# Optimization experiments

Hardware: AMD Instinct MI355X
Metric: run time of the kernel (lower is better)

Reference implementation:

```python
import jax, jax.numpy as jnp
import numpy as np

L = 5           # num_layer
D = 128         # emb_dim
N = 100_000     # num nodes
E = 1_600_000   # num edges
EDGE_F = 7      # raw edge feature dim
BN_EPS = 1e-5


def batchnorm(z, gamma, beta):
    # BatchNorm1d in training-style normalization: biased batch mean/var over axis 0
    mu = z.mean(axis=0)
    var = z.var(axis=0)
    return gamma * (z - mu) * jax.lax.rsqrt(var + BN_EPS) + beta


def setup_inputs() -> dict:
    key = jax.random.key(0)
    ks = jax.random.split(key, 16)
    s = 0.05
    return {
        "x": jnp.zeros((N,), jnp.int32),                               # Embedding(1, D) indices
        "edge_index": jax.random.randint(ks[0], (2, E), 0, N, jnp.int32),
        "edge_attr": jax.random.normal(ks[1], (E, EDGE_F), jnp.float32),
        "node_emb": jax.random.normal(ks[2], (1, D), jnp.float32) * s,
        "We": jax.random.normal(ks[3], (L, EDGE_F, D), jnp.float32) * s,   # edge_encoder weight
        "be": jax.random.normal(ks[4], (L, D), jnp.float32) * s,
        "eps": jnp.zeros((L,), jnp.float32),                               # GIN eps, init 0
        "W1": jax.random.normal(ks[5], (L, D, 2 * D), jnp.float32) * s,
        "b1": jax.random.normal(ks[6], (L, 2 * D), jnp.float32) * s,
        "g1": jnp.ones((L, 2 * D), jnp.float32),                           # mlp inner BN gamma
        "bt1": jnp.zeros((L, 2 * D), jnp.float32),                         # mlp inner BN beta
        "W2": jax.random.normal(ks[7], (L, 2 * D, D), jnp.float32) * s,
        "b2": jax.random.normal(ks[8], (L, D), jnp.float32) * s,
        "gbn": jnp.ones((L, D), jnp.float32),                              # outer BN gamma
        "bbn": jnp.zeros((L, D), jnp.float32),                             # outer BN beta
    }


def reference(x, edge_index, edge_attr, node_emb, We, be, eps, W1, b1, g1, bt1, W2, b2, gbn, bbn):
    # node encoder (Embedding with vocab=1)
    h = node_emb[x]                       # [N, D]
    src, dst = edge_index[0], edge_index[1]
    for l in range(L):
        # edge embedding + GIN message: relu(x_j + edge_emb), scatter-add at dst
        ee = edge_attr @ We[l] + be[l]                       # [E, D]
        msg = jax.nn.relu(h[src] + ee)                       # gather + add + relu
        agg = jax.ops.segment_sum(msg, dst, num_segments=N)  # scatter-add
        out = (1.0 + eps[l]) * h + agg                       # [N, D]
        # mlp: Linear(D,2D) -> BN -> ReLU -> Linear(2D,D)
        z = batchnorm(out @ W1[l] + b1[l], g1[l], bt1[l])
        z = jax.nn.relu(z) @ W2[l] + b2[l]
        # outer BatchNorm; dropout is identity in eval mode
        h = batchnorm(z, gbn[l], bbn[l])
        if l < L - 1:
            h = jax.nn.relu(h)
    return h
```

## Files before the change

kernel.cpp:

```cpp
#include <hip/hip_runtime.h>
#include <cstddef>

#define NN 100000
#define NE 1600000
#define D 128
#define D2 256
#define EF 7
#define NL 5
#define BN_EPS 1e-5f
#define GW 12500
#define SCAN_NB ((NN + 1023) / 1024)

typedef unsigned short ushort_t;
typedef __attribute__((ext_vector_type(8))) _Float16 f16x8;
typedef __attribute__((ext_vector_type(2))) _Float16 h2v;
typedef __attribute__((ext_vector_type(4))) float f32x4;

__device__ __forceinline__ void atomAddF(float* p, float v) { unsafeAtomicAdd(p, v); }

__device__ __forceinline__ ushort_t f2h(float f) {
    return __builtin_bit_cast(ushort_t, (_Float16)f);
}
__device__ __forceinline__ unsigned pk2h(float lo, float hi) {
    return (unsigned)f2h(lo) | ((unsigned)f2h(hi) << 16);
}
__device__ __forceinline__ float h2f(unsigned u16) {
    return (float)__builtin_bit_cast(_Float16, (ushort_t)(u16 & 0xFFFFu));
}
__device__ __forceinline__ h2v u2h2(unsigned u) { return __builtin_bit_cast(h2v, u); }

__global__ __launch_bounds__(256)
void hist_kernel(const int* __restrict__ ei, int* __restrict__ counts)
{
    const int e = blockIdx.x * 256 + threadIdx.x;
    if (e < NE) atomicAdd(&counts[ei[NE + e]], 1);
}

__global__ __launch_bounds__(256)
void scanA_kernel(const int* __restrict__ counts, int* __restrict__ bsum)
{
    __shared__ int sred[256];
    const int t = threadIdx.x;
    const int base = blockIdx.x * 1024 + t * 4;
    int s = 0;
    #pragma unroll
    for (int j = 0; j < 4; ++j) { const int i = base + j; if (i < NN) s += counts[i]; }
    sred[t] = s;
    __syncthreads();
    for (int off = 128; off > 0; off >>= 1) {
        if (t < off) sred[t] += sred[t + off];
        __syncthreads();
    }
    if (t == 0) bsum[blockIdx.x] = sred[0];
}

__global__ __launch_bounds__(128)
void scanB_kernel(const int* __restrict__ bsum, int* __restrict__ bbase,
                  int* __restrict__ offs)
{
    __shared__ int ss[128];
    const int t = threadIdx.x;
    const int v = (t < SCAN_NB) ? bsum[t] : 0;
    ss[t] = v;
    __syncthreads();
    for (int off = 1; off < 128; off <<= 1) {
        int u = 0;
        if (t >= off) u = ss[t - off];
        __syncthreads();
        ss[t] += u;
        __syncthreads();
    }
    if (t < SCAN_NB) bbase[t] = ss[t] - v;
    if (t == 0) offs[NN] = NE;
}

__global__ __launch_bounds__(256)
void scanC_kernel(const int* __restrict__ counts, const int* __restrict__ bbase,
                  int* __restrict__ offs, int* __restrict__ offmut)
{
    __shared__ int sts[256];
    const int t = threadIdx.x;
    const int base = blockIdx.x * 1024 + t * 4;
    int c[4];
    int s = 0;
    #pragma unroll
    for (int j = 0; j < 4; ++j) {
        const int i = base + j;
        c[j] = (i < NN) ? counts[i] : 0;
        s += c[j];
    }
    sts[t] = s;
    __syncthreads();
    for (int off = 1; off < 256; off <<= 1) {
        int u = 0;
        if (t >= off) u = sts[t - off];
        __syncthreads();
        sts[t] += u;
        __syncthreads();
    }
    int run = bbase[blockIdx.x] + sts[t] - s;
    #pragma unroll
    for (int j = 0; j < 4; ++j) {
        const int i = base + j;
        if (i < NN) { offs[i] = run; offmut[i] = run; run += c[j]; }
    }
}

__global__ __launch_bounds__(256)
void scatter_kernel(const int* __restrict__ ei, const float* __restrict__ ea,
                    int* __restrict__ offmut, int* __restrict__ sSrc,
                    ushort_t* __restrict__ eaH)
{
    const int e = blockIdx.x * 256 + threadIdx.x;
    if (e < NE) {
        const int dst = ei[NE + e];
        const int pos = atomicAdd(&offmut[dst], 1);
        sSrc[pos] = ei[e];
        const float* eap = &ea[(size_t)e * EF];
        const unsigned o0 = pk2h(eap[0], eap[1]);
        const unsigned o1 = pk2h(eap[2], eap[3]);
        const unsigned o2 = pk2h(eap[4], eap[5]);
        const unsigned o3 = pk2h(eap[6], 0.f);
        *(uint4*)&eaH[(size_t)pos * 8] = make_uint4(o0, o1, o2, o3);
    }
}

__global__ __launch_bounds__(256)
void wconv_kernel(const float* __restrict__ W1, const float* __restrict__ W2,
                  ushort_t* __restrict__ W1t, ushort_t* __restrict__ W2t)
{
    const int idx = blockIdx.x * 256 + threadIdx.x;
    const int per = D * D2;
    if (idx < NL * per) {
        const int l = idx / per, r = idx % per;
        const int k1 = r / D2, n1 = r % D2;
        W1t[(size_t)l * per + n1 * D + k1] = f2h(W1[idx]);
        const int k2 = r / D, n2 = r % D;
        W2t[(size_t)l * per + n2 * D2 + k2] = f2h(W2[idx]);
    }
}

template<int L0>
__global__ __launch_bounds__(256)
void gather_kernel(const int* __restrict__ offs, const int* __restrict__ sSrc,
                   const ushort_t* __restrict__ eaH,
                   const float* __restrict__ We, const float* __restrict__ be,
                   const ushort_t* __restrict__ z2H, const float* __restrict__ stats2p,
                   const float* __restrict__ gbn, const float* __restrict__ bbn,
                   const float* __restrict__ h0, const float* __restrict__ epsp,
                   ushort_t* __restrict__ xinH, float* __restrict__ xsum)
{
    __shared__ __align__(16) float sCS[4][D];
    const int lane = threadIdx.x & 63;
    const int w = threadIdx.x >> 6;
    const int wid = blockIdx.x * 4 + w;

    const float2* We2 = (const float2*)We;
    const unsigned* hU = (const unsigned*)z2H;
    unsigned* xU = (unsigned*)xinH;
    h2v wP[EF];
    #pragma unroll
    for (int k = 0; k < EF; ++k) {
        const float2 wf = We2[k * 64 + lane];
        wP[k] = (h2v){(_Float16)wf.x, (_Float16)wf.y};
    }
    h2v beP;
    {
        const float2 bf = ((const float2*)be)[lane];
        beP = (h2v){(_Float16)bf.x, (_Float16)bf.y};
    }
    float2 h0v = {0.f, 0.f};
    h2v h0P = (h2v){(_Float16)0.f, (_Float16)0.f};
    h2v aP = (h2v){(_Float16)0.f, (_Float16)0.f};
    h2v cP = (h2v){(_Float16)0.f, (_Float16)0.f};
    if (L0) {
        h0v = ((const float2*)h0)[lane];
        h0P = (h2v){(_Float16)h0v.x, (_Float16)h0v.y};
    } else {
        const float inv = 1.0f / (float)NN;
        const int c0i = 2 * lane, c1i = 2 * lane + 1;
        const float mu0 = stats2p[c0i] * inv;
        const float mu1 = stats2p[c1i] * inv;
        const float v0 = fmaf(-mu0, mu0, stats2p[D + c0i] * inv);
        const float v1 = fmaf(-mu1, mu1, stats2p[D + c1i] * inv);
        const float a0 = gbn[c0i] * rsqrtf(v0 + BN_EPS);
        const float a1 = gbn[c1i] * rsqrtf(v1 + BN_EPS);
        const float c0 = fmaf(-a0, mu0, bbn[c0i]);
        const float c1 = fmaf(-a1, mu1, bbn[c1i]);
        aP = (h2v){(_Float16)a0, (_Float16)a1};
        cP = (h2v){(_Float16)c0, (_Float16)c1};
    }
    const float epsv = 1.0f + *epsp;
    const h2v zz = (h2v){(_Float16)0.f, (_Float16)0.f};

    int p4[8], e4[8];
    #pragma unroll
    for (int i = 0; i < 8; ++i) {
        const int n = wid + i * GW;
        p4[i] = __builtin_amdgcn_readfirstlane(offs[n]);
        e4[i] = __builtin_amdgcn_readfirstlane(offs[n + 1]);
    }
    int mx = 0;
    #pragma unroll
    for (int i = 0; i < 8; ++i) mx = max(mx, e4[i] - p4[i]);

    float2 acc[8];
    #pragma unroll
    for (int i = 0; i < 8; ++i) acc[i] = (float2){0.f, 0.f};

    for (int j = 0; j < mx; ++j) {
        unsigned hwd[8];
        uint4 ev4[8];
        bool on[8];
        #pragma unroll
        for (int i = 0; i < 8; ++i) {
            on[i] = p4[i] < e4[i];
            if (on[i]) {
                ev4[i] = *(const uint4*)&eaH[(size_t)p4[i] * 8];
                if (!L0) {
                    const int src = sSrc[p4[i]];
                    hwd[i] = hU[(src << 6) + lane];
                }
            }
        }
        #pragma unroll
        for (int i = 0; i < 8; ++i) {
            if (on[i]) {
                const h2v e01 = u2h2(ev4[i].x);
                const h2v e23 = u2h2(ev4[i].y);
                const h2v e45 = u2h2(ev4[i].z);
                const h2v e6x = u2h2(ev4[i].w);
                h2v m = beP;
                m = __builtin_elementwise_fma(__builtin_shufflevector(e01, e01, 0, 0), wP[0], m);
                m = __builtin_elementwise_fma(__builtin_shufflevector(e01, e01, 1, 1), wP[1], m);
                m = __builtin_elementwise_fma(__builtin_shufflevector(e23, e23, 0, 0), wP[2], m);
                m = __builtin_elementwise_fma(__builtin_shufflevector(e23, e23, 1, 1), wP[3], m);
                m = __builtin_elementwise_fma(__builtin_shufflevector(e45, e45, 0, 0), wP[4], m);
                m = __builtin_elementwise_fma(__builtin_shufflevector(e45, e45, 1, 1), wP[5], m);
                m = __builtin_elementwise_fma(__builtin_shufflevector(e6x, e6x, 0, 0), wP[6], m);
                h2v hh;
                if (L0) hh = h0P;
                else hh = __builtin_elementwise_max(
                         __builtin_elementwise_fma(aP, u2h2(hwd[i]), cP), zz);
                const h2v r = __builtin_elementwise_max(m + hh, zz);
                acc[i].x += (float)r.x;
                acc[i].y += (float)r.y;
                ++p4[i];
            }
        }
    }

    float2 cs = {0.f, 0.f};
    #pragma unroll
    for (int i = 0; i < 8; ++i) {
        const int n = wid + i * GW;
        float2 hs;
        if (L0) hs = h0v;
        else {
            const h2v hz = __builtin_elementwise_max(
                __builtin_elementwise_fma(aP, u2h2(hU[(n << 6) + lane]), cP), zz);
            hs.x = (float)hz.x; hs.y = (float)hz.y;
        }
        float2 a = acc[i];
        a.x = fmaf(epsv, hs.x, a.x);
        a.y = fmaf(epsv, hs.y, a.y);
        cs.x += a.x; cs.y += a.y;
        xU[(n << 6) + lane] = pk2h(a.x, a.y);
    }
    sCS[w][2 * lane] = cs.x;
    sCS[w][2 * lane + 1] = cs.y;
    __syncthreads();
    if (threadIdx.x < D) {
        atomAddF(&xsum[threadIdx.x],
                 sCS[0][threadIdx.x] + sCS[1][threadIdx.x] +
                 sCS[2][threadIdx.x] + sCS[3][threadIdx.x]);
    }
}

__global__ __launch_bounds__(256, 2)
void mm1_kernel(const ushort_t* __restrict__ xinH, const float* __restrict__ xsum,
                const ushort_t* __restrict__ W1t,
                ushort_t* __restrict__ z1H, float* __restrict__ stats)
{
    __shared__ __align__(16) ushort_t sA[64 * 256];
    __shared__ __align__(16) float sM[D];
    const int t = threadIdx.x;
    if (t < D) sM[t] = xsum[t] * (1.0f / (float)NN);
    const int i0 = blockIdx.x * 64;
    const int lane = t & 63, w = t >> 6;
    const int nb = w * 64;

    f16x8 bfr[4][4];
    #pragma unroll
    for (int nt = 0; nt < 4; ++nt)
        #pragma unroll
        for (int ks = 0; ks < 4; ++ks) {
            const int n = nb + nt * 16 + (lane & 15);
            const int k = ks * 32 + (lane >> 4) * 8;
            bfr[nt][ks] = *(const f16x8*)&W1t[n * D + k];
        }
    __syncthreads();

    #pragma unroll
    for (int p = 0; p < 4; ++p) {
        const int linear = p * 256 + t;
        const int row = linear >> 4, ch = linear & 15;
        const int gi = i0 + row;
        unsigned oo[4] = {0, 0, 0, 0};
        if (gi < NN) {
            const uint4 v = *(const uint4*)&xinH[(size_t)gi * D + ch * 8];
            const unsigned uu[4] = {v.x, v.y, v.z, v.w};
            #pragma unroll
            for (int j2 = 0; j2 < 4; ++j2) {
                const int c0 = ch * 8 + j2 * 2;
                oo[j2] = pk2h(h2f(uu[j2]) - sM[c0], h2f(uu[j2] >> 16) - sM[c0 + 1]);
            }
        }
        unsigned boff = (unsigned)(row * 256 + ch * 16);
        boff ^= (unsigned)((row & 7) << 4);
        *(uint4*)((char*)sA + boff) = make_uint4(oo[0], oo[1], oo[2], oo[3]);
    }
    __syncthreads();

    f32x4 acc[4][4];
    #pragma unroll
    for (int a = 0; a < 4; ++a)
        #pragma unroll
        for (int b = 0; b < 4; ++b) acc[a][b] = (f32x4){0.f, 0.f, 0.f, 0.f};

    #pragma unroll
    for (int mt = 0; mt < 4; ++mt) {
        f16x8 af[4];
        #pragma unroll
        for (int ks = 0; ks < 4; ++ks) {
            const int row = mt * 16 + (lane & 15);
            unsigned boff = (unsigned)(row * 256 + ks * 64 + (lane >> 4) * 16);
            boff ^= (unsigned)((row & 7) << 4);
            af[ks] = *(const f16x8*)((const char*)sA + boff);
        }
        #pragma unroll
        for (int nt = 0; nt < 4; ++nt)
            #pragma unroll
            for (int ks = 0; ks < 4; ++ks)
                acc[mt][nt] = __builtin_amdgcn_mfma_f32_16x16x32_f16(af[ks], bfr[nt][ks], acc[mt][nt], 0, 0, 0);
    }

    float s[4], q[4];
    #pragma unroll
    for (int nt = 0; nt < 4; ++nt) { s[nt] = 0.f; q[nt] = 0.f; }
    #pragma unroll
    for (int nt = 0; nt < 4; ++nt)
        #pragma unroll
        for (int mt = 0; mt < 4; ++mt)
            #pragma unroll
            for (int r = 0; r < 4; ++r) {
                const int i = i0 + mt * 16 + (lane >> 4) * 4 + r;
                if (i < NN) {
                    const float v = acc[mt][nt][r];
                    s[nt] += v; q[nt] = fmaf(v, v, q[nt]);
                }
            }
    #pragma unroll
    for (int nt = 0; nt < 4; ++nt) {
        s[nt] += __shfl_xor(s[nt], 16, 64); s[nt] += __shfl_xor(s[nt], 32, 64);
        q[nt] += __shfl_xor(q[nt], 16, 64); q[nt] += __shfl_xor(q[nt], 32, 64);
    }
    if (lane < 16) {
        #pragma unroll
        for (int nt = 0; nt < 4; ++nt) {
            const int n = nb + nt * 16 + lane;
            atomAddF(&stats[n], s[nt]);
            atomAddF(&stats[D2 + n], q[nt]);
        }
    }

    __syncthreads();
    #pragma unroll
    for (int nt = 0; nt < 4; ++nt)
        #pragma unroll
        for (int mt = 0; mt < 4; ++mt)
            #pragma unroll
            for (int r = 0; r < 4; ++r) {
                const int row = mt * 16 + (lane >> 4) * 4 + r;
                const int col = nb + nt * 16 + (lane & 15);
                const unsigned byte = (unsigned)(row * 512 + col * 2) ^ ((unsigned)(row & 7) << 4);
                *(ushort_t*)((char*)sA + byte) = f2h(acc[mt][nt][r]);
            }
    __syncthreads();
    {
        const int row = t >> 2;
        const int gi = i0 + row;
        const int cb = (t & 3) * 64;
        if (gi < NN) {
            #pragma unroll
            for (int c = 0; c < 8; ++c) {
                const unsigned byte = (unsigned)(row * 512 + (cb + c * 8) * 2) ^ ((unsigned)(row & 7) << 4);
                const uint4 v = *(const uint4*)((const char*)sA + byte);
                *(uint4*)&z1H[(size_t)gi * D2 + cb + c * 8] = v;
            }
        }
    }
}

__global__ __launch_bounds__(256, 2)
void mm2_kernel(const ushort_t* __restrict__ z1H, const float* __restrict__ stats1,
                const float* __restrict__ g1, const float* __restrict__ bt1,
                const ushort_t* __restrict__ W2t,
                ushort_t* __restrict__ z2H, float* __restrict__ stats2)
{
    __shared__ __align__(16) ushort_t sA[64 * 256];
    __shared__ __align__(16) float sAff[2 * D2];
    __shared__ __align__(16) float sYm[D2];
    const int t = threadIdx.x;
    {
        const float inv = 1.0f / (float)NN;
        const float mu = stats1[t] * inv;
        const float var = fmaf(-mu, mu, stats1[D2 + t] * inv);
        const float a = g1[t] * rsqrtf(var + BN_EPS);
        sAff[t] = a;
        sAff[D2 + t] = fmaf(-a, mu, bt1[t]);
        const float m0 = bt1[t];
        const float sg = fabsf(g1[t]);
        float ym;
        if (sg > 1e-20f) {
            const float r = m0 / sg;
            const float Ph = 0.5f * (1.0f + erff(r * 0.70710678f));
            const float ph = 0.39894228f * expf(-0.5f * r * r);
            ym = m0 * Ph + sg * ph;
        } else {
            ym = fmaxf(m0, 0.f);
        }
        sYm[t] = ym;
    }
    const int i0 = blockIdx.x * 64;
    const int lane = t & 63, w = t >> 6;
    const int nb = w * 32;

    f16x8 bfr[2][8];
    #pragma unroll
    for (int nt = 0; nt < 2; ++nt)
        #pragma unroll
        for (int ks = 0; ks < 8; ++ks) {
            const int n = nb + nt * 16 + (lane & 15);
            const int k = ks * 32 + (lane >> 4) * 8;
            bfr[nt][ks] = *(const f16x8*)&W2t[n * D2 + k];
        }
    __syncthreads();

    #pragma unroll
    for (int p = 0; p < 8; ++p) {
        const int linear = p * 256 + t;
        const int row = linear >> 5, ch = linear & 31;
        const int gi = i0 + row;
        unsigned oo[4] = {0, 0, 0, 0};
        if (gi < NN) {
            const uint4 v = *(const uint4*)&z1H[(size_t)gi * D2 + ch * 8];
            const unsigned uu[4] = {v.x, v.y, v.z, v.w};
            #pragma unroll
            for (int j2 = 0; j2 < 4; ++j2) {
                const int c0 = ch * 8 + j2 * 2;
                float lo = h2f(uu[j2]);
                float hi = h2f(uu[j2] >> 16);
                lo = fmaxf(fmaf(sAff[c0], lo, sAff[D2 + c0]), 0.f) - sYm[c0];
                hi = fmaxf(fmaf(sAff[c0 + 1], hi, sAff[D2 + c0 + 1]), 0.f) - sYm[c0 + 1];
                oo[j2] = pk2h(lo, hi);
            }
        }
        unsigned boff = (unsigned)(row * 512 + ch * 16);
        boff ^= (unsigned)((row & 7) << 4);
        *(uint4*)((char*)sA + boff) = make_uint4(oo[0], oo[1], oo[2], oo[3]);
    }
    __syncthreads();

    f32x4 acc[4][2];
    #pragma unroll
    for (int a = 0; a < 4; ++a)
        #pragma unroll
        for (int b = 0; b < 2; ++b) acc[a][b] = (f32x4){0.f, 0.f, 0.f, 0.f};

    #pragma unroll
    for (int mt = 0; mt < 4; ++mt) {
        f16x8 af[8];
        #pragma unroll
        for (int ks = 0; ks < 8; ++ks) {
            const int row = mt * 16 + (lane & 15);
            unsigned boff = (unsigned)(row * 512 + ks * 64 + (lane >> 4) * 16);
            boff ^= (unsigned)((row & 7) << 4);
            af[ks] = *(const f16x8*)((const char*)sA + boff);
        }
        #pragma unroll
        for (int nt = 0; nt < 2; ++nt)
            #pragma unroll
            for (int ks = 0; ks < 8; ++ks)
                acc[mt][nt] = __builtin_amdgcn_mfma_f32_16x16x32_f16(af[ks], bfr[nt][ks], acc[mt][nt], 0, 0, 0);
    }

    float s[2], q[2];
    #pragma unroll
    for (int nt = 0; nt < 2; ++nt) { s[nt] = 0.f; q[nt] = 0.f; }
    #pragma unroll
    for (int nt = 0; nt < 2; ++nt)
        #pragma unroll
        for (int mt = 0; mt < 4; ++mt)
            #pragma unroll
            for (int r = 0; r < 4; ++r) {
                const int i = i0 + mt * 16 + (lane >> 4) * 4 + r;
                if (i < NN) {
                    const float v = acc[mt][nt][r];
                    s[nt] += v; q[nt] = fmaf(v, v, q[nt]);
                }
            }
    #pragma unroll
    for (int nt = 0; nt < 2; ++nt) {
        s[nt] += __shfl_xor(s[nt], 16, 64); s[nt] += __shfl_xor(s[nt], 32, 64);
        q[nt] += __shfl_xor(q[nt], 16, 64); q[nt] += __shfl_xor(q[nt], 32, 64);
    }
    if (lane < 16) {
        #pragma unroll
        for (int nt = 0; nt < 2; ++nt) {
            const int n = nb + nt * 16 + lane;
            atomAddF(&stats2[n], s[nt]);
            atomAddF(&stats2[D + n], q[nt]);
        }
    }

    __syncthreads();
    #pragma unroll
    for (int nt = 0; nt < 2; ++nt)
        #pragma unroll
        for (int mt = 0; mt < 4; ++mt)
            #pragma unroll
            for (int r = 0; r < 4; ++r) {
                const int row = mt * 16 + (lane >> 4) * 4 + r;
                const int col = nb + nt * 16 + (lane & 15);
                const unsigned byte = (unsigned)(row * 256 + col * 2) ^ ((unsigned)(row & 7) << 4);
                *(ushort_t*)((char*)sA + byte) = f2h(acc[mt][nt][r]);
            }
    __syncthreads();
    {
        const int row = t >> 2;
        const int gi = i0 + row;
        const int cb = (t & 3) * 32;
        if (gi < NN) {
            #pragma unroll
            for (int c = 0; c < 4; ++c) {
                const unsigned byte = (unsigned)(row * 256 + (cb + c * 8) * 2) ^ ((unsigned)(row & 7) << 4);
                const uint4 v = *(const uint4*)((const char*)sA + byte);
                *(uint4*)&z2H[(size_t)gi * D + cb + c * 8] = v;
            }
        }
    }
}

__global__ __launch_bounds__(256)
void act_kernel(const ushort_t* __restrict__ z2H, const float* __restrict__ stats2,
                const float* __restrict__ g, const float* __restrict__ bt,
                float* __restrict__ out)
{
    __shared__ float sA[D], sC[D];
    const int t = threadIdx.x;
    if (t < D) {
        const float inv = 1.0f / (float)NN;
        const float mu = stats2[t] * inv;
        const float var = fmaf(-mu, mu, stats2[D + t] * inv);
        const float a = g[t] * rsqrtf(var + BN_EPS);
        sA[t] = a;
        sC[t] = fmaf(-a, mu, bt[t]);
    }
    __syncthreads();
    const int idx = blockIdx.x * 256 + t;
    if (idx < NN * D / 4) {
        const int d0 = (idx * 4) & (D - 1);
        const uint2 v = *(const uint2*)&z2H[(size_t)idx * 4];
        float4 o;
        o.x = fmaf(sA[d0 + 0], h2f(v.x),       sC[d0 + 0]);
        o.y = fmaf(sA[d0 + 1], h2f(v.x >> 16), sC[d0 + 1]);
        o.z = fmaf(sA[d0 + 2], h2f(v.y),       sC[d0 + 2]);
        o.w = fmaf(sA[d0 + 3], h2f(v.y >> 16), sC[d0 + 3]);
        *(float4*)&out[(size_t)idx * 4] = o;
    }
}

extern "C" void kernel_launch(void* const* d_in, const int* in_sizes, int n_in,
                              void* d_out, int out_size, void* d_ws, size_t ws_size,
                              hipStream_t stream)
{
    (void)in_sizes; (void)n_in; (void)out_size; (void)ws_size;
    const int*   ei       = (const int*)d_in[1];
    const float* ea       = (const float*)d_in[2];
    const float* node_emb = (const float*)d_in[3];
    const float* We       = (const float*)d_in[4];
    const float* be       = (const float*)d_in[5];
    const float* eps      = (const float*)d_in[6];
    const float* W1       = (const float*)d_in[7];
    const float* g1       = (const float*)d_in[9];
    const float* bt1      = (const float*)d_in[10];
    const float* W2       = (const float*)d_in[11];
    const float* gbn      = (const float*)d_in[13];
    const float* bbn      = (const float*)d_in[14];
    float* out = (float*)d_out;

    char* base = (char*)d_ws;
    size_t off = 0;
    auto alloc = [&](size_t bytes) -> void* {
        void* p = base + off;
        off = (off + bytes + 255) & ~(size_t)255;
        return p;
    };
    ushort_t* xinH   = (ushort_t*)alloc((size_t)NN * D * 2);
    ushort_t* z1H    = (ushort_t*)alloc((size_t)NN * D2 * 2);
    ushort_t* z2H    = (ushort_t*)alloc((size_t)NN * D * 2);
    ushort_t* W1t    = (ushort_t*)alloc((size_t)NL * D * D2 * 2);
    ushort_t* W2t    = (ushort_t*)alloc((size_t)NL * D * D2 * 2);
    float*    red    = (float*)alloc((size_t)NL * 896 * sizeof(float));
    int*      counts = (int*)alloc((NN + 1) * sizeof(int));
    int*      offs   = (int*)alloc((NN + 1) * sizeof(int));
    int*      offmut = (int*)alloc(NN * sizeof(int));
    int*      bsum   = (int*)alloc(SCAN_NB * sizeof(int));
    int*      bbase  = (int*)alloc(SCAN_NB * sizeof(int));
    int*      sSrc   = (int*)alloc((size_t)NE * sizeof(int));
    ushort_t* eaH    = (ushort_t*)alloc((size_t)NE * 8 * 2);

    hipMemsetAsync(counts, 0, (NN + 1) * sizeof(int), stream);
    hipMemsetAsync(red, 0, (size_t)NL * 896 * sizeof(float), stream);
    hist_kernel<<<(NE + 255) / 256, 256, 0, stream>>>(ei, counts);
    scanA_kernel<<<SCAN_NB, 256, 0, stream>>>(counts, bsum);
    scanB_kernel<<<1, 128, 0, stream>>>(bsum, bbase, offs);
    scanC_kernel<<<SCAN_NB, 256, 0, stream>>>(counts, bbase, offs, offmut);
    scatter_kernel<<<(NE + 255) / 256, 256, 0, stream>>>(ei, ea, offmut, sSrc, eaH);
    wconv_kernel<<<(NL * D * D2 + 255) / 256, 256, 0, stream>>>(W1, W2, W1t, W2t);

    for (int l = 0; l < NL; ++l) {
        float* redl   = red + (size_t)l * 896;
        float* stats1 = redl;
        float* stats2 = redl + 512;
        float* xsum   = redl + 768;
        if (l == 0) {
            gather_kernel<1><<<GW / 4, 256, 0, stream>>>(offs, sSrc, eaH,
                We + l * EF * D, be + l * D,
                z2H, nullptr, nullptr, nullptr,
                node_emb, eps + l, xinH, xsum);
        } else {
            const float* stats2p = red + (size_t)(l - 1) * 896 + 512;
            gather_kernel<0><<<GW / 4, 256, 0, stream>>>(offs, sSrc, eaH,
                We + l * EF * D, be + l * D,
                z2H, stats2p, gbn + (l - 1) * D, bbn + (l - 1) * D,
                node_emb, eps + l, xinH, xsum);
        }
        mm1_kernel<<<(NN + 63) / 64, 256, 0, stream>>>(xinH, xsum, W1t + (size_t)l * D * D2,
                                                       z1H, stats1);
        mm2_kernel<<<(NN + 63) / 64, 256, 0, stream>>>(z1H, stats1, g1 + l * D2, bt1 + l * D2,
                                                       W2t + (size_t)l * D * D2,
                                                       z2H, stats2);
    }
    act_kernel<<<(NN * D / 4 + 255) / 256, 256, 0, stream>>>(
        z2H, red + (size_t)(NL - 1) * 896 + 512, gbn + (NL - 1) * D, bbn + (NL - 1) * D, out);
}
```

Baseline: 1.560 ms.

## Sort nodes by in-degree so each gather wave handles similar-degree nodes

Adds a counting sort of nodes by in-degree (capped at 64 buckets) that builds a permutation. Each gather wave now takes 8 consecutive nodes from the sorted order, so the per-wave loop bound set by the largest degree wastes fewer idle iterations. Wave indices are scrambled with a multiplicative hash so heavy and light groups spread across blocks. The cost is three small preprocessing kernels plus one more indirection, and node reads and writes become scattered instead of strided.

Result: slower. 1.716 ms (+10.0%).

```diff
diff --git a/kernel.cpp b/kernel.cpp
--- a/kernel.cpp
+++ b/kernel.cpp
@@ -10,6 +10,7 @@
 #define BN_EPS 1e-5f
 #define GW 12500
 #define SCAN_NB ((NN + 1023) / 1024)
+#define DB 64
 
 typedef unsigned short ushort_t;
 typedef __attribute__((ext_vector_type(8))) _Float16 f16x8;
@@ -103,6 +104,65 @@
     for (int j = 0; j < 4; ++j) {
         const int i = base + j;
         if (i < NN) { offs[i] = run; offmut[i] = run; run += c[j]; }
+    }
+}
+
+__global__ __launch_bounds__(256)
+void dhistL_kernel(const int* __restrict__ counts, int* __restrict__ bh)
+{
+    __shared__ int lh[DB];
+    const int t = threadIdx.x;
+    if (t < DB) lh[t] = 0;
+    __syncthreads();
+    const int base = blockIdx.x * 1024 + t * 4;
+    #pragma unroll
+    for (int j = 0; j < 4; ++j) {
+        const int i = base + j;
+        if (i < NN) atomicAdd(&lh[min(counts[i], DB - 1)], 1);
+    }
+    __syncthreads();
+    if (t < DB) bh[t * SCAN_NB + blockIdx.x] = lh[t];
+}
+
+__global__ __launch_bounds__(DB)
+void dscan2_kernel(const int* __restrict__ bh, int* __restrict__ gb)
+{
+    __shared__ int tot[DB];
+    __shared__ int gdb[DB];
+    const int d = threadIdx.x;
+    int run = 0;
+    for (int b = 0; b < SCAN_NB; ++b) run += bh[d * SCAN_NB + b];
+    tot[d] = run;
+    __syncthreads();
+    if (d == 0) {
+        int r = 0;
+        for (int k = 0; k < DB; ++k) { gdb[k] = r; r += tot[k]; }
+    }
+    __syncthreads();
+    run = gdb[d];
+    for (int b = 0; b < SCAN_NB; ++b) {
+        const int v = bh[d * SCAN_NB + b];
+        gb[d * SCAN_NB + b] = run;
+        run += v;
+    }
+}
+
+__global__ __launch_bounds__(256)
+void dpermL_kernel(const int* __restrict__ counts, const int* __restrict__ gb,
+                   int* __restrict__ perm)
+{
+    __shared__ int cur[DB];
+    const int t = threadIdx.x;
+    if (t < DB) cur[t] = gb[t * SCAN_NB + blockIdx.x];
+    __syncthreads();
+    const int base = blockIdx.x * 1024 + t * 4;
+    #pragma unroll
+    for (int j = 0; j < 4; ++j) {
+        const int i = base + j;
+        if (i < NN) {
+            const int r = atomicAdd(&cur[min(counts[i], DB - 1)], 1);
+            perm[r] = i;
+        }
     }
 }
 
@@ -143,7 +203,7 @@
 template<int L0>
 __global__ __launch_bounds__(256)
 void gather_kernel(const int* __restrict__ offs, const int* __restrict__ sSrc,
-                   const ushort_t* __restrict__ eaH,
+                   const ushort_t* __restrict__ eaH, const int* __restrict__ perm,
                    const float* __restrict__ We, const float* __restrict__ be,
                    const ushort_t* __restrict__ z2H, const float* __restrict__ stats2p,
                    const float* __restrict__ gbn, const float* __restrict__ bbn,
@@ -154,6 +214,7 @@
     const int lane = threadIdx.x & 63;
     const int w = threadIdx.x >> 6;
     const int wid = blockIdx.x * 4 + w;
+    const int wids = (int)(((long long)wid * 9973) % GW);
 
     const float2* We2 = (const float2*)We;
     const unsigned* hU = (const unsigned*)z2H;
@@ -193,12 +254,12 @@
     const float epsv = 1.0f + *epsp;
     const h2v zz = (h2v){(_Float16)0.f, (_Float16)0.f};
 
-    int p4[8], e4[8];
+    int nd[8], p4[8], e4[8];
     #pragma unroll
     for (int i = 0; i < 8; ++i) {
-        const int n = wid + i * GW;
-        p4[i] = __builtin_amdgcn_readfirstlane(offs[n]);
-        e4[i] = __builtin_amdgcn_readfirstlane(offs[n + 1]);
+        nd[i] = __builtin_amdgcn_readfirstlane(perm[wids * 8 + i]);
+        p4[i] = __builtin_amdgcn_readfirstlane(offs[nd[i]]);
+        e4[i] = __builtin_amdgcn_readfirstlane(offs[nd[i] + 1]);
     }
     int mx = 0;
     #pragma unroll
@@ -253,7 +314,7 @@
     float2 cs = {0.f, 0.f};
     #pragma unroll
     for (int i = 0; i < 8; ++i) {
-        const int n = wid + i * GW;
+        const int n = nd[i];
         float2 hs;
         if (L0) hs = h0v;
         else {
@@ -618,6 +679,9 @@
     int*      offmut = (int*)alloc(NN * sizeof(int));
     int*      bsum   = (int*)alloc(SCAN_NB * sizeof(int));
     int*      bbase  = (int*)alloc(SCAN_NB * sizeof(int));
+    int*      bh     = (int*)alloc((size_t)DB * SCAN_NB * sizeof(int));
+    int*      gb     = (int*)alloc((size_t)DB * SCAN_NB * sizeof(int));
+    int*      perm   = (int*)alloc(NN * sizeof(int));
     int*      sSrc   = (int*)alloc((size_t)NE * sizeof(int));
     ushort_t* eaH    = (ushort_t*)alloc((size_t)NE * 8 * 2);
 
@@ -627,6 +691,9 @@
     scanA_kernel<<<SCAN_NB, 256, 0, stream>>>(counts, bsum);
     scanB_kernel<<<1, 128, 0, stream>>>(bsum, bbase, offs);
     scanC_kernel<<<SCAN_NB, 256, 0, stream>>>(counts, bbase, offs, offmut);
+    dhistL_kernel<<<SCAN_NB, 256, 0, stream>>>(counts, bh);
+    dscan2_kernel<<<1, DB, 0, stream>>>(bh, gb);
+    dpermL_kernel<<<SCAN_NB, 256, 0, stream>>>(counts, gb, perm);
     scatter_kernel<<<(NE + 255) / 256, 256, 0, stream>>>(ei, ea, offmut, sSrc, eaH);
     wconv_kernel<<<(NL * D * D2 + 255) / 256, 256, 0, stream>>>(W1, W2, W1t, W2t);
 
@@ -636,13 +703,13 @@
         float* stats2 = redl + 512;
         float* xsum   = redl + 768;
         if (l == 0) {
-            gather_kernel<1><<<GW / 4, 256, 0, stream>>>(offs, sSrc, eaH,
+            gather_kernel<1><<<GW / 4, 256, 0, stream>>>(offs, sSrc, eaH, perm,
                 We + l * EF * D, be + l * D,
                 z2H, nullptr, nullptr, nullptr,
                 node_emb, eps + l, xinH, xsum);
         } else {
             const float* stats2p = red + (size_t)(l - 1) * 896 + 512;
-            gather_kernel<0><<<GW / 4, 256, 0, stream>>>(offs, sSrc, eaH,
+            gather_kernel<0><<<GW / 4, 256, 0, stream>>>(offs, sSrc, eaH, perm,
                 We + l * EF * D, be + l * D,
                 z2H, stats2p, gbn + (l - 1) * D, bbn + (l - 1) * D,
                 node_emb, eps + l, xinH, xsum);
```
